# Kernel optimization log

Hardware: AMD Instinct MI355X
Metric: run time of the kernel (lower is better)

The kernel has to match this reference:

```python
import jax, jax.numpy as jnp
import numpy as np

EPS = 1e-06

def feature_map(x):
    # ELU + 1 feature map (default in LinearAttention)
    return jax.nn.elu(x) + 1.0

def setup_inputs() -> dict:
    key = jax.random.key(0)
    kq, kk, kv = jax.random.split(key, 3)
    N, L, H, D = 4, 8192, 16, 64
    queries = jax.random.normal(kq, (N, L, H, D), dtype=jnp.float32)
    keys = jax.random.normal(kk, (N, L, H, D), dtype=jnp.float32)
    values = jax.random.normal(kv, (N, L, H, D), dtype=jnp.float32)
    return {"queries": queries, "keys": keys, "values": values}

def reference(queries, keys, values):
    # Q, K: [N, L, H, D] after ELU+1 feature map
    Q = feature_map(queries)
    K = feature_map(keys)
    # KV state: [N, H, D, M]
    KV = jnp.einsum('nshd,nshm->nhdm', K, values)
    # normalizer: Z[n,l,h] = 1 / (Q . sum_s K + eps)
    Z = 1.0 / (jnp.einsum('nlhd,nhd->nlh', Q, K.sum(axis=1)) + EPS)
    # NOTE: faithful to original: KV (nhdm) is labeled 'nhmd' in the einsum,
    # i.e. KV is used transposed on its last two axes (requires D == M).
    V = jnp.einsum('nlhd,nhmd,nlh->nlhm', Q, KV, Z)
    return V
```

## Files before the change

kernel.cpp:

```cpp
#include <hip/hip_runtime.h>
#include <hip/hip_bf16.h>

#define LDIM 8192
#define HDIM 16
#define DDIM 64
#define NHEADPAIR 64
#define ROWSTRIDE 1024
#define KVSZ 4160
#define EPSF 1e-6f
#define TROWS 32
#define CHUNKS 32
#define RPB 256
#define NT 8

typedef float f32x4 __attribute__((ext_vector_type(4)));
typedef short s16x8 __attribute__((ext_vector_type(8)));

__device__ __forceinline__ float featmap(float x) {
    return x > 0.0f ? x + 1.0f : __expf(x);
}

__device__ __forceinline__ unsigned int pack_bf16x2(float a, float b) {
    union { __hip_bfloat162 h; unsigned int u; } x;
    x.h = __float22bfloat162_rn(make_float2(a, b));
    return x.u;
}

__device__ __forceinline__ int swz(int d) { return ((d >> 3) & 3) << 2; }

__global__ __launch_bounds__(256) void kv_mfma_kernel(
    const float* __restrict__ Kp, const float* __restrict__ Vp,
    float* __restrict__ part)
{
    __shared__ unsigned int KT[2][4][1024];
    __shared__ unsigned int VT[2][4][1024];

    const int bq   = blockIdx.x;
    const int n    = bq >> 2;
    const int hq   = bq & 3;
    const int ch   = blockIdx.y;
    const int t    = threadIdx.x;
    const int wave = t >> 6;
    const int lane = t & 63;

    const bool isK = (t < 128);
    const int  u   = t & 127;
    const int  dg  = u & 7;
    const int  rp  = u >> 3;
    const float* Sp = isK ? Kp : Vp;
    const size_t base0 = (((size_t)n * LDIM + (size_t)ch * RPB + 2 * rp) * ROWSTRIDE)
                       + hq * 256 + dg * 8;

    const int fr = lane & 15;
    const int fk = lane >> 4;

    f32x4 acc[4][4];
    f32x4 zac[4];
#pragma unroll
    for (int b = 0; b < 4; ++b) {
        zac[b] = (f32x4){0.f, 0.f, 0.f, 0.f};
#pragma unroll
        for (int mb = 0; mb < 4; ++mb) acc[b][mb] = (f32x4){0.f, 0.f, 0.f, 0.f};
    }
    s16x8 ones;
#pragma unroll
    for (int i = 0; i < 8; ++i) ones[i] = (short)0x3F80;

    float4 st[4][4];

#pragma unroll
    for (int hh = 0; hh < 4; ++hh) {
        const float* S = Sp + base0 + hh * 64;
        st[hh][0] = *(const float4*)(S);
        st[hh][1] = *(const float4*)(S + 4);
        st[hh][2] = *(const float4*)(S + ROWSTRIDE);
        st[hh][3] = *(const float4*)(S + ROWSTRIDE + 4);
    }
#pragma unroll
    for (int hh = 0; hh < 4; ++hh) {
        unsigned int* T = isK ? &KT[0][hh][0] : &VT[0][hh][0];
        const float* a = (const float*)&st[hh][0];
        const float* b = (const float*)&st[hh][2];
#pragma unroll
        for (int j = 0; j < 8; ++j) {
            const int d = dg * 8 + j;
            float fe = a[j], fo = b[j];
            if (isK) { fe = featmap(fe); fo = featmap(fo); }
            T[d * 16 + (rp ^ swz(d))] = pack_bf16x2(fe, fo);
        }
    }
    __syncthreads();

    int buf = 0;
    for (int tt = 0; tt < NT; ++tt) {
        const bool more = (tt + 1 < NT);
        if (more) {
#pragma unroll
            for (int hh = 0; hh < 4; ++hh) {
                const float* S = Sp + base0
                               + (size_t)(tt + 1) * TROWS * ROWSTRIDE + hh * 64;
                st[hh][0] = *(const float4*)(S);
                st[hh][1] = *(const float4*)(S + 4);
                st[hh][2] = *(const float4*)(S + ROWSTRIDE);
                st[hh][3] = *(const float4*)(S + ROWSTRIDE + 4);
            }
        }

        {
            s16x8 A[4];
#pragma unroll
            for (int b = 0; b < 4; ++b) {
                const int d = b * 16 + fr;
                A[b] = *(const s16x8*)&KT[buf][wave][d * 16 + ((fk * 4) ^ swz(d))];
            }
#pragma unroll
            for (int b = 0; b < 4; ++b)
                zac[b] = __builtin_amdgcn_mfma_f32_16x16x32_bf16(A[b], ones, zac[b], 0, 0, 0);
#pragma unroll
            for (int mb = 0; mb < 4; ++mb) {
                const int m = mb * 16 + fr;
                s16x8 B = *(const s16x8*)&VT[buf][wave][m * 16 + ((fk * 4) ^ swz(m))];
#pragma unroll
                for (int b = 0; b < 4; ++b)
                    acc[b][mb] = __builtin_amdgcn_mfma_f32_16x16x32_bf16(A[b], B, acc[b][mb], 0, 0, 0);
            }
        }

        if (more) {
#pragma unroll
            for (int hh = 0; hh < 4; ++hh) {
                unsigned int* T = isK ? &KT[buf ^ 1][hh][0] : &VT[buf ^ 1][hh][0];
                const float* a = (const float*)&st[hh][0];
                const float* b = (const float*)&st[hh][2];
#pragma unroll
                for (int j = 0; j < 8; ++j) {
                    const int d = dg * 8 + j;
                    float fe = a[j], fo = b[j];
                    if (isK) { fe = featmap(fe); fo = featmap(fo); }
                    T[d * 16 + (rp ^ swz(d))] = pack_bf16x2(fe, fo);
                }
            }
        }
        __syncthreads();
        buf ^= 1;
    }

    const int nh = n * 16 + hq * 4 + wave;
    float* p = part + ((size_t)nh * CHUNKS + ch) * KVSZ;
#pragma unroll
    for (int b = 0; b < 4; ++b)
#pragma unroll
        for (int mb = 0; mb < 4; ++mb)
#pragma unroll
            for (int reg = 0; reg < 4; ++reg)
                p[(b * 16 + fk * 4 + reg) * 64 + mb * 16 + fr] = acc[b][mb][reg];
    if (fr == 0)
#pragma unroll
        for (int b = 0; b < 4; ++b)
#pragma unroll
            for (int reg = 0; reg < 4; ++reg)
                p[4096 + b * 16 + fk * 4 + reg] = zac[b][reg];
}

__global__ __launch_bounds__(256) void kv_reduce_kernel(
    const float* __restrict__ part, unsigned short* __restrict__ kvh)
{
    const int nh = blockIdx.y;
    const int e  = blockIdx.x * 256 + threadIdx.x;
    if (e >= KVSZ) return;
    float s = 0.0f;
    for (int c = 0; c < CHUNKS; ++c)
        s += part[((size_t)nh * CHUNKS + c) * KVSZ + e];
    union { __hip_bfloat16 h; unsigned short u; } cv;
    cv.h = __float2bfloat16(s);
    kvh[(size_t)nh * KVSZ + e] = cv.u;
}

__global__ __launch_bounds__(256) void attn_mfma_kernel(
    const float* __restrict__ Qp, const unsigned short* __restrict__ kvh,
    float* __restrict__ out)
{
    __shared__ unsigned int kvU[64][36];
    __shared__ unsigned int ksU[36];
    __shared__ unsigned int qU[128][36];

    const int nh = blockIdx.y;
    const int n  = nh >> 4;
    const int h  = nh & 15;
    const int t  = threadIdx.x;

    {
        const unsigned int* kvg = (const unsigned int*)(kvh + (size_t)nh * KVSZ);
        const int r  = t >> 2;
        const int c0 = (t & 3) * 8;
        uint4 x = *(const uint4*)(kvg + r * 32 + c0);
        uint4 y = *(const uint4*)(kvg + r * 32 + c0 + 4);
        *(uint4*)&kvU[r][c0]     = x;
        *(uint4*)&kvU[r][c0 + 4] = y;
        if (t < 32) ksU[t] = kvg[2048 + t];
    }

    {
        const int qr = t >> 1;
        const float* qg = Qp + ((((size_t)n * LDIM) + (size_t)blockIdx.x * 128 + qr)
                                * HDIM + h) * DDIM + (t & 1) * 32;
        unsigned int q[16];
#pragma unroll
        for (int j = 0; j < 8; ++j) {
            float4 f = *(const float4*)(qg + j * 4);
            q[2 * j]     = pack_bf16x2(featmap(f.x), featmap(f.y));
            q[2 * j + 1] = pack_bf16x2(featmap(f.z), featmap(f.w));
        }
        uint4* dst = (uint4*)&qU[qr][(t & 1) * 16];
        dst[0] = make_uint4(q[0],  q[1],  q[2],  q[3]);
        dst[1] = make_uint4(q[4],  q[5],  q[6],  q[7]);
        dst[2] = make_uint4(q[8],  q[9],  q[10], q[11]);
        dst[3] = make_uint4(q[12], q[13], q[14], q[15]);
    }
    __syncthreads();

    const int wave = t >> 6;
    const int lane = t & 63;
    const int fr = lane & 15;
    const int fk = lane >> 4;

    s16x8 bF[4][2], kF[2];
#pragma unroll
    for (int mt = 0; mt < 4; ++mt)
#pragma unroll
        for (int kk = 0; kk < 2; ++kk)
            bF[mt][kk] = *(const s16x8*)&kvU[mt * 16 + fr][kk * 16 + fk * 4];
#pragma unroll
    for (int kk = 0; kk < 2; ++kk)
        kF[kk] = *(const s16x8*)&ksU[kk * 16 + fk * 4];

    f32x4 acc[2][4];
    f32x4 zac[2];
#pragma unroll
    for (int lt = 0; lt < 2; ++lt) {
        zac[lt] = (f32x4){0.f, 0.f, 0.f, 0.f};
#pragma unroll
        for (int mt = 0; mt < 4; ++mt) acc[lt][mt] = (f32x4){0.f, 0.f, 0.f, 0.f};
    }

#pragma unroll
    for (int kk = 0; kk < 2; ++kk) {
#pragma unroll
        for (int lt = 0; lt < 2; ++lt) {
            s16x8 A = *(const s16x8*)&qU[wave * 32 + lt * 16 + fr][kk * 16 + fk * 4];
            zac[lt] = __builtin_amdgcn_mfma_f32_16x16x32_bf16(A, kF[kk], zac[lt], 0, 0, 0);
#pragma unroll
            for (int mt = 0; mt < 4; ++mt)
                acc[lt][mt] = __builtin_amdgcn_mfma_f32_16x16x32_bf16(
                    A, bF[mt][kk], acc[lt][mt], 0, 0, 0);
        }
    }

#pragma unroll
    for (int lt = 0; lt < 2; ++lt) {
#pragma unroll
        for (int reg = 0; reg < 4; ++reg) {
            const int row = blockIdx.x * 128 + wave * 32 + lt * 16 + fk * 4 + reg;
            const float z = 1.0f / (zac[lt][reg] + EPSF);
            float* orow = out + (((size_t)n * LDIM + row) * HDIM + h) * DDIM;
#pragma unroll
            for (int mt = 0; mt < 4; ++mt)
                orow[mt * 16 + fr] = acc[lt][mt][reg] * z;
        }
    }
}

extern "C" void kernel_launch(void* const* d_in, const int* in_sizes, int n_in,
                              void* d_out, int out_size, void* d_ws, size_t ws_size,
                              hipStream_t stream) {
    const float* Q = (const float*)d_in[0];
    const float* K = (const float*)d_in[1];
    const float* V = (const float*)d_in[2];
    float* out = (float*)d_out;
    float* ws  = (float*)d_ws;

    float* part = ws;
    unsigned short* kvh = (unsigned short*)(ws + (size_t)NHEADPAIR * CHUNKS * KVSZ);

    dim3 g1(16, CHUNKS);
    kv_mfma_kernel<<<g1, 256, 0, stream>>>(K, V, part);
    dim3 gr((KVSZ + 255) / 256, NHEADPAIR);
    kv_reduce_kernel<<<gr, 256, 0, stream>>>(part, kvh);
    dim3 g2(LDIM / 128, NHEADPAIR);
    attn_mfma_kernel<<<g2, 256, 0, stream>>>(Q, kvh, out);
}
```

Baseline: 149.8 us.

## Replace pipelined KV kernel with one-shot per-head chunk kernel

The KV-state kernel now launches one block per (chunk, head) with 128 rows per block. It loads the whole chunk into padded shared memory once and splits the D dimension across waves, replacing the double-buffered multi-tile loop where each wave handled its own head. This gives 4096 blocks instead of 512, for more parallelism and less per-block serial work. The cost is twice as many partial sums written and read by the reduce kernel, and global loads that are no longer overlapped with MFMA inside a block.

```diff
diff --git a/kernel.cpp b/kernel.cpp
--- a/kernel.cpp
+++ b/kernel.cpp
@@ -8,10 +8,9 @@
 #define ROWSTRIDE 1024
 #define KVSZ 4160
 #define EPSF 1e-6f
-#define TROWS 32
-#define CHUNKS 32
-#define RPB 256
-#define NT 8
+#define CHUNKS 64
+#define RPB 128
+#define LROW 68
 
 typedef float f32x4 __attribute__((ext_vector_type(4)));
 typedef short s16x8 __attribute__((ext_vector_type(8)));
@@ -28,17 +27,17 @@
 
 __device__ __forceinline__ int swz(int d) { return ((d >> 3) & 3) << 2; }
 
-__global__ __launch_bounds__(256) void kv_mfma_kernel(
+__global__ __launch_bounds__(256) void kv_oneshot_kernel(
     const float* __restrict__ Kp, const float* __restrict__ Vp,
     float* __restrict__ part)
 {
-    __shared__ unsigned int KT[2][4][1024];
-    __shared__ unsigned int VT[2][4][1024];
-
-    const int bq   = blockIdx.x;
-    const int n    = bq >> 2;
-    const int hq   = bq & 3;
-    const int ch   = blockIdx.y;
+    __shared__ unsigned int KT[64 * LROW];
+    __shared__ unsigned int VT[64 * LROW];
+
+    const int ch   = blockIdx.x;
+    const int nh   = blockIdx.y;
+    const int n    = nh >> 4;
+    const int h    = nh & 15;
     const int t    = threadIdx.x;
     const int wave = t >> 6;
     const int lane = t & 63;
@@ -48,118 +47,72 @@
     const int  dg  = u & 7;
     const int  rp  = u >> 3;
     const float* Sp = isK ? Kp : Vp;
-    const size_t base0 = (((size_t)n * LDIM + (size_t)ch * RPB + 2 * rp) * ROWSTRIDE)
-                       + hq * 256 + dg * 8;
-
-    const int fr = lane & 15;
-    const int fk = lane >> 4;
-
-    f32x4 acc[4][4];
-    f32x4 zac[4];
-#pragma unroll
-    for (int b = 0; b < 4; ++b) {
-        zac[b] = (f32x4){0.f, 0.f, 0.f, 0.f};
-#pragma unroll
-        for (int mb = 0; mb < 4; ++mb) acc[b][mb] = (f32x4){0.f, 0.f, 0.f, 0.f};
-    }
-    s16x8 ones;
-#pragma unroll
-    for (int i = 0; i < 8; ++i) ones[i] = (short)0x3F80;
+    const size_t base = (((size_t)n * LDIM + (size_t)ch * RPB) * HDIM + h) * DDIM
+                      + dg * 8;
 
     float4 st[4][4];
-
-#pragma unroll
-    for (int hh = 0; hh < 4; ++hh) {
-        const float* S = Sp + base0 + hh * 64;
-        st[hh][0] = *(const float4*)(S);
-        st[hh][1] = *(const float4*)(S + 4);
-        st[hh][2] = *(const float4*)(S + ROWSTRIDE);
-        st[hh][3] = *(const float4*)(S + ROWSTRIDE + 4);
-    }
-#pragma unroll
-    for (int hh = 0; hh < 4; ++hh) {
-        unsigned int* T = isK ? &KT[0][hh][0] : &VT[0][hh][0];
-        const float* a = (const float*)&st[hh][0];
-        const float* b = (const float*)&st[hh][2];
+#pragma unroll
+    for (int i = 0; i < 4; ++i) {
+        const int sp = rp + 16 * i;
+        const float* g = Sp + base + (size_t)(2 * sp) * ROWSTRIDE;
+        st[i][0] = *(const float4*)(g);
+        st[i][1] = *(const float4*)(g + 4);
+        st[i][2] = *(const float4*)(g + ROWSTRIDE);
+        st[i][3] = *(const float4*)(g + ROWSTRIDE + 4);
+    }
+
+    unsigned int* T = isK ? KT : VT;
+#pragma unroll
+    for (int i = 0; i < 4; ++i) {
+        const int sp = rp + 16 * i;
+        const float* a = (const float*)&st[i][0];
+        const float* b = (const float*)&st[i][2];
 #pragma unroll
         for (int j = 0; j < 8; ++j) {
             const int d = dg * 8 + j;
             float fe = a[j], fo = b[j];
             if (isK) { fe = featmap(fe); fo = featmap(fo); }
-            T[d * 16 + (rp ^ swz(d))] = pack_bf16x2(fe, fo);
+            T[d * LROW + (sp ^ swz(d))] = pack_bf16x2(fe, fo);
         }
     }
     __syncthreads();
 
-    int buf = 0;
-    for (int tt = 0; tt < NT; ++tt) {
-        const bool more = (tt + 1 < NT);
-        if (more) {
-#pragma unroll
-            for (int hh = 0; hh < 4; ++hh) {
-                const float* S = Sp + base0
-                               + (size_t)(tt + 1) * TROWS * ROWSTRIDE + hh * 64;
-                st[hh][0] = *(const float4*)(S);
-                st[hh][1] = *(const float4*)(S + 4);
-                st[hh][2] = *(const float4*)(S + ROWSTRIDE);
-                st[hh][3] = *(const float4*)(S + ROWSTRIDE + 4);
-            }
-        }
-
-        {
-            s16x8 A[4];
-#pragma unroll
-            for (int b = 0; b < 4; ++b) {
-                const int d = b * 16 + fr;
-                A[b] = *(const s16x8*)&KT[buf][wave][d * 16 + ((fk * 4) ^ swz(d))];
-            }
-#pragma unroll
-            for (int b = 0; b < 4; ++b)
-                zac[b] = __builtin_amdgcn_mfma_f32_16x16x32_bf16(A[b], ones, zac[b], 0, 0, 0);
-#pragma unroll
-            for (int mb = 0; mb < 4; ++mb) {
-                const int m = mb * 16 + fr;
-                s16x8 B = *(const s16x8*)&VT[buf][wave][m * 16 + ((fk * 4) ^ swz(m))];
-#pragma unroll
-                for (int b = 0; b < 4; ++b)
-                    acc[b][mb] = __builtin_amdgcn_mfma_f32_16x16x32_bf16(A[b], B, acc[b][mb], 0, 0, 0);
-            }
-        }
-
-        if (more) {
-#pragma unroll
-            for (int hh = 0; hh < 4; ++hh) {
-                unsigned int* T = isK ? &KT[buf ^ 1][hh][0] : &VT[buf ^ 1][hh][0];
-                const float* a = (const float*)&st[hh][0];
-                const float* b = (const float*)&st[hh][2];
-#pragma unroll
-                for (int j = 0; j < 8; ++j) {
-                    const int d = dg * 8 + j;
-                    float fe = a[j], fo = b[j];
-                    if (isK) { fe = featmap(fe); fo = featmap(fo); }
-                    T[d * 16 + (rp ^ swz(d))] = pack_bf16x2(fe, fo);
-                }
-            }
-        }
-        __syncthreads();
-        buf ^= 1;
-    }
-
-    const int nh = n * 16 + hq * 4 + wave;
+    const int fr = lane & 15;
+    const int fk = lane >> 4;
+    const int d0 = wave * 16;
+
+    f32x4 acc[4];
+    f32x4 zac = (f32x4){0.f, 0.f, 0.f, 0.f};
+#pragma unroll
+    for (int mb = 0; mb < 4; ++mb) acc[mb] = (f32x4){0.f, 0.f, 0.f, 0.f};
+    s16x8 ones;
+#pragma unroll
+    for (int i = 0; i < 8; ++i) ones[i] = (short)0x3F80;
+
+    const int dA = d0 + fr;
+#pragma unroll
+    for (int kk = 0; kk < 4; ++kk) {
+        const int slot = kk * 16 + fk * 4;
+        s16x8 A = *(const s16x8*)&KT[dA * LROW + (slot ^ swz(dA))];
+        zac = __builtin_amdgcn_mfma_f32_16x16x32_bf16(A, ones, zac, 0, 0, 0);
+#pragma unroll
+        for (int mb = 0; mb < 4; ++mb) {
+            const int m = mb * 16 + fr;
+            s16x8 B = *(const s16x8*)&VT[m * LROW + (slot ^ swz(m))];
+            acc[mb] = __builtin_amdgcn_mfma_f32_16x16x32_bf16(A, B, acc[mb], 0, 0, 0);
+        }
+    }
+
     float* p = part + ((size_t)nh * CHUNKS + ch) * KVSZ;
 #pragma unroll
-    for (int b = 0; b < 4; ++b)
-#pragma unroll
-        for (int mb = 0; mb < 4; ++mb)
-#pragma unroll
-            for (int reg = 0; reg < 4; ++reg)
-                p[(b * 16 + fk * 4 + reg) * 64 + mb * 16 + fr] = acc[b][mb][reg];
+    for (int mb = 0; mb < 4; ++mb)
+#pragma unroll
+        for (int reg = 0; reg < 4; ++reg)
+            p[(d0 + fk * 4 + reg) * 64 + mb * 16 + fr] = acc[mb][reg];
     if (fr == 0)
 #pragma unroll
-        for (int b = 0; b < 4; ++b)
-#pragma unroll
-            for (int reg = 0; reg < 4; ++reg)
-                p[4096 + b * 16 + fk * 4 + reg] = zac[b][reg];
+        for (int reg = 0; reg < 4; ++reg)
+            p[4096 + d0 + fk * 4 + reg] = zac[reg];
 }
 
 __global__ __launch_bounds__(256) void kv_reduce_kernel(
@@ -282,8 +235,8 @@
     float* part = ws;
     unsigned short* kvh = (unsigned short*)(ws + (size_t)NHEADPAIR * CHUNKS * KVSZ);
 
-    dim3 g1(16, CHUNKS);
-    kv_mfma_kernel<<<g1, 256, 0, stream>>>(K, V, part);
+    dim3 g1(CHUNKS, NHEADPAIR);
+    kv_oneshot_kernel<<<g1, 256, 0, stream>>>(K, V, part);
     dim3 gr((KVSZ + 255) / 256, NHEADPAIR);
     kv_reduce_kernel<<<gr, 256, 0, stream>>>(part, kvh);
     dim3 g2(LDIM / 128, NHEADPAIR);
```

Result: slower. 159.3 us (+6.3%).
